# Kernel tuning notes

Measured on AMD Instinct MI355X. Metric: run time of the kernel, lower is better.

Reference implementation:

```python
import jax, jax.numpy as jnp
import numpy as np

V, D_EMB, H, N_LAYERS = 50257, 512, 1024, 2
B, T = 8, 512


def setup_inputs() -> dict:
    key = jax.random.key(0)
    ks = jax.random.split(key, 9)
    s = 0.02
    return {
        "x": jax.random.randint(ks[0], (B, T), 0, V),
        "y": jax.random.randint(ks[1], (B, T), 0, V),
        "E": jax.random.normal(ks[2], (V, D_EMB), jnp.float32) * s,
        "Wih0": jax.random.normal(ks[3], (D_EMB, H), jnp.float32) * s,
        "Whh0": jax.random.normal(ks[4], (H, H), jnp.float32) * s,
        "Wih1": jax.random.normal(ks[5], (H, H), jnp.float32) * s,
        "Whh1": jax.random.normal(ks[6], (H, H), jnp.float32) * s,
        "Wfc": jax.random.normal(ks[7], (H, V), jnp.float32) * s,
        "bfc": jnp.zeros((V,), jnp.float32),
    }


def _rnn_layer(x_tbd, Wih, Whh):
    # x_tbd: (T, B, Din) time-major; tanh Elman cell, no bias.
    h0 = jnp.zeros((x_tbd.shape[1], Whh.shape[0]), x_tbd.dtype)

    def step(h, x_t):
        h_new = jnp.tanh(x_t @ Wih + h @ Whh)
        return h_new, h_new

    h_last, ys = jax.lax.scan(step, h0, x_tbd)
    return ys, h_last  # ys: (T, B, H)


def reference(x, y, E, Wih0, Whh0, Wih1, Whh1, Wfc, bfc):
    xe = E[x]                              # (B, T, D_EMB) embedding gather
    xs = jnp.swapaxes(xe, 0, 1)            # (T, B, D_EMB)
    ys0, _ = _rnn_layer(xs, Wih0, Whh0)    # layer 0
    ys1, _ = _rnn_layer(ys0, Wih1, Whh1)   # layer 1
    feats = jnp.swapaxes(ys1, 0, 1)        # (B, T, H)
    logits = feats @ Wfc + bfc             # (B, T, V)
    # cross_entropy with ignore_index=-1 (mean over valid tokens)
    flat = logits.reshape(-1, logits.shape[-1])
    yf = y.reshape(-1)
    valid = yf != -1
    y_safe = jnp.where(valid, yf, 0)
    logp = jax.nn.log_softmax(flat, axis=-1)
    nll = -jnp.take_along_axis(logp, y_safe[:, None], axis=-1)[:, 0]
    loss = jnp.sum(jnp.where(valid, nll, 0.0)) / jnp.maximum(valid.sum(), 1)
    return logits, loss
```

## Files before the change

### kernel.cpp

```cpp
#include <hip/hip_runtime.h>


#define H_DIM 1024
#define B_SZ 8
#define T_SZ 512
#define V_SZ 50257
#define V_PAD 50304
#define NTILES 12576

typedef __attribute__((ext_vector_type(8))) short bf16x8;
typedef __attribute__((ext_vector_type(4))) float f32x4;

__device__ __forceinline__ unsigned short f2bf(float f) {
  unsigned int u = __float_as_uint(f);
  u += 0x7fffu + ((u >> 16) & 1u);
  return (unsigned short)(u >> 16);
}
__device__ __forceinline__ float bf2f(unsigned short h) {
  return __uint_as_float(((unsigned int)h) << 16);
}
__device__ __forceinline__ float ftanh(float x) {
  float e = __expf(2.f * x);
  return 1.f - 2.f / (e + 1.f);
}
__device__ __forceinline__ int aload32(const int* p) {
  return __hip_atomic_load(p, __ATOMIC_RELAXED, __HIP_MEMORY_SCOPE_AGENT);
}
__device__ __forceinline__ void astore32(unsigned int* p, unsigned int v) {
  __hip_atomic_store(p, v, __ATOMIC_RELAXED, __HIP_MEMORY_SCOPE_AGENT);
}
__device__ __forceinline__ void astore32i(int* p, int v) {
  __hip_atomic_store(p, v, __ATOMIC_RELAXED, __HIP_MEMORY_SCOPE_AGENT);
}
__device__ __forceinline__ unsigned long long aload64(const void* p) {
  return __hip_atomic_load((const unsigned long long*)p, __ATOMIC_RELAXED,
                           __HIP_MEMORY_SCOPE_AGENT);
}
__device__ __forceinline__ void astore64(void* p, unsigned long long v) {
  __hip_atomic_store((unsigned long long*)p, v, __ATOMIC_RELAXED,
                     __HIP_MEMORY_SCOPE_AGENT);
}
__device__ __forceinline__ void gload_lds16(const void* g, void* l) {
  __builtin_amdgcn_global_load_lds(
      (const __attribute__((address_space(1))) void*)g,
      (__attribute__((address_space(3))) void*)l, 16, 0, 0);
}

__global__ __launch_bounds__(256) void k_transpose(
    const float* __restrict__ in, unsigned short* __restrict__ out,
    int K, int N, int Npad)
{
  __shared__ float tile[32][33];
  const int n0 = blockIdx.x * 32, k0 = blockIdx.y * 32;
  const int tx = threadIdx.x, ty = threadIdx.y;
#pragma unroll
  for (int jj = 0; jj < 4; ++jj) {
    int k = k0 + ty + jj * 8, n = n0 + tx;
    tile[ty + jj * 8][tx] = (n < N) ? in[(size_t)k * N + n] : 0.f;
  }
  __syncthreads();
#pragma unroll
  for (int jj = 0; jj < 4; ++jj) {
    int n = n0 + ty + jj * 8, k = k0 + tx;
    if (n < Npad) out[(size_t)n * K + k] = f2bf((n < N) ? tile[tx][ty + jj * 8] : 0.f);
  }
}

__global__ __launch_bounds__(128) void k_embed(
    const int* __restrict__ x, const float* __restrict__ E,
    unsigned short* __restrict__ xe)
{
  const int r = blockIdx.x;
  const int t = r >> 3, b = r & 7;
  const int tok = x[b * T_SZ + t];
  const float4 v = ((const float4*)(E + (size_t)tok * 512))[threadIdx.x];
  ushort4 o;
  o.x = f2bf(v.x); o.y = f2bf(v.y); o.z = f2bf(v.z); o.w = f2bf(v.w);
  *((ushort4*)(xe + (size_t)r * 512) + threadIdx.x) = o;
}

template <bool BF16_OUT, bool BIAS>
__global__ __launch_bounds__(256) void k_gemm(
    const unsigned short* __restrict__ A, const unsigned short* __restrict__ Bt,
    void* __restrict__ Cout, const float* __restrict__ bias,
    int Nvalid, int K, int lda, int ldb, int ldc)
{
  __shared__ unsigned short As[8192];
  __shared__ unsigned short Bs[8192];
  const int tid = threadIdx.x;
  const int n0 = blockIdx.x * 128;
  const int m0 = blockIdx.y * 128;
  const int lane = tid & 63;
  const int wv = tid >> 6;
  const int wm = wv >> 1, wn = wv & 1;
  const int ln = lane & 15, cc = lane >> 4;
  f32x4 acc[4][4] = {};
  const int rr = tid >> 3;
  const int cb = (tid & 7) << 4;

  for (int kb = 0; kb < K; kb += 64) {
    __syncthreads();
#pragma unroll
    for (int is = 0; is < 4; ++is) {
      int r = is * 32 + rr;
      int sb = cb ^ ((r & 7) << 4);
      gload_lds16((const char*)(A + (size_t)(m0 + r) * lda + kb) + sb,
                  &As[(is * 32 + 8 * wv) * 64]);
    }
#pragma unroll
    for (int is = 0; is < 4; ++is) {
      int r = is * 32 + rr;
      int sb = cb ^ ((r & 7) << 4);
      gload_lds16((const char*)(Bt + (size_t)(n0 + r) * ldb + kb) + sb,
                  &Bs[(is * 32 + 8 * wv) * 64]);
    }
    __syncthreads();
#pragma unroll
    for (int kk = 0; kk < 2; ++kk) {
      bf16x8 af[4], bfr[4];
      const int kslot = kk * 64 + cc * 16;
#pragma unroll
      for (int mi = 0; mi < 4; ++mi) {
        int ra = wm * 64 + mi * 16 + ln;
        af[mi] = *(const bf16x8*)((const char*)As + ra * 128 + (kslot ^ ((ra & 7) << 4)));
      }
#pragma unroll
      for (int ni = 0; ni < 4; ++ni) {
        int rb = wn * 64 + ni * 16 + ln;
        bfr[ni] = *(const bf16x8*)((const char*)Bs + rb * 128 + (kslot ^ ((rb & 7) << 4)));
      }
#pragma unroll
      for (int mi = 0; mi < 4; ++mi)
#pragma unroll
        for (int ni = 0; ni < 4; ++ni)
          acc[mi][ni] = __builtin_amdgcn_mfma_f32_16x16x32_bf16(af[mi], bfr[ni], acc[mi][ni], 0, 0, 0);
    }
  }
#pragma unroll
  for (int ni = 0; ni < 4; ++ni) {
    const int col = n0 + wn * 64 + ni * 16 + ln;
    const bool cok = col < Nvalid;
    float bv = 0.f;
    if (BIAS && cok) bv = bias[col];
#pragma unroll
    for (int mi = 0; mi < 4; ++mi) {
#pragma unroll
      for (int i = 0; i < 4; ++i) {
        if (cok) {
          const int rowg = m0 + wm * 64 + mi * 16 + cc * 4 + i;
          if (BF16_OUT)
            ((unsigned short*)Cout)[(size_t)rowg * ldc + col] = f2bf(acc[mi][ni][i]);
          else
            ((float*)Cout)[(size_t)rowg * ldc + col] = acc[mi][ni][i] + bv;
        }
      }
    }
  }
}

template <int NQ>
__device__ __forceinline__ void gatherN(const uint2* __restrict__ sl,
    unsigned want, char* __restrict__ lds, int lane, int rowoff)
{
  unsigned long long v[NQ];
  for (;;) {
    bool ok = true;
#pragma unroll
    for (int q = 0; q < NQ; ++q)
      v[q] = aload64(sl + q * 64 + lane);
#pragma unroll
    for (int q = 0; q < NQ; ++q)
      ok &= ((unsigned)v[q] == want);
    if (__all(ok)) break;
  }
#pragma unroll
  for (int q = 0; q < NQ; ++q) {
    const int j = q * 64 + lane;
    const int row = rowoff + (j >> 9), kp = j & 511;
    *(unsigned*)(lds + ((row * 2048 + kp * 4) ^ ((row & 7) << 4))) =
        (unsigned)(v[q] >> 32);
  }
}

__device__ __forceinline__ void load_bw(bf16x8* bw, const float* W, int cc, int col)
{
#pragma unroll
  for (int kc = 0; kc < 32; ++kc) {
    const float* wp = W + (size_t)(kc * 32 + cc * 8) * H_DIM + col;
    bf16x8 v;
#pragma unroll
    for (int q = 0; q < 8; ++q) v[q] = (short)f2bf(wp[(size_t)q * H_DIM]);
    bw[kc] = v;
  }
}

__device__ __forceinline__ f32x4 mfma_k1024(const char* hs, const bf16x8* bw,
                                            int cc, int r)
{
  f32x4 ac0 = {}, ac1 = {};
  const int swz = r << 4;
#pragma unroll
  for (int kc = 0; kc < 32; kc += 2) {
    bf16x8 a0 = *(const bf16x8*)(hs + r * 2048 + ((kc * 64 + cc * 16) ^ swz));
    bf16x8 a1 = *(const bf16x8*)(hs + r * 2048 + (((kc + 1) * 64 + cc * 16) ^ swz));
    ac0 = __builtin_amdgcn_mfma_f32_16x16x32_bf16(a0, bw[kc], ac0, 0, 0, 0);
    ac1 = __builtin_amdgcn_mfma_f32_16x16x32_bf16(a1, bw[kc + 1], ac1, 0, 0, 0);
  }
  return ac0 + ac1;
}

__device__ void rec0(const unsigned short* U0, const float* Whh0,
    uint2* h0ring, const int* prog, char* smem, int wg)
{
  __builtin_amdgcn_s_setprio(1);
  const int tid = threadIdx.x, lane = tid & 63, wv = tid >> 6;
  const int ln = lane & 15, cc = lane >> 4, r = ln & 7;
  const int col = wg * 64 + wv * 16 + ln;
  char* stage = smem;
  bf16x8 bw[32];
  load_bw(bw, Whh0, cc, col);
#pragma unroll 1
  for (int t = 0; t < T_SZ; ++t) {
    unsigned short uva[4] = {0, 0, 0, 0};
    if (cc < 2) {
#pragma unroll
      for (int i = 0; i < 4; ++i)
        uva[i] = U0[(size_t)(t * B_SZ + cc * 4 + i) * H_DIM + col];
    }
    gatherN<16>(h0ring + ((t + 3) & 3) * 4096 + wv * 1024, (unsigned)t,
                stage, lane, wv * 2);
    __syncthreads();
    f32x4 ac = mfma_k1024(stage, bw, cc, r);
    __syncthreads();
    float hv[4] = {0.f, 0.f, 0.f, 0.f};
    if (cc < 2) {
#pragma unroll
      for (int i = 0; i < 4; ++i) hv[i] = ftanh(ac[i] + bf2f(uva[i]));
    }
    unsigned wpk[4];
#pragma unroll
    for (int i = 0; i < 4; ++i) {
      float pv = __shfl_xor(hv[i], 1);
      wpk[i] = (unsigned)f2bf(hv[i]) | ((unsigned)f2bf(pv) << 16);
    }
    if (t >= 4) {
      const int* pp = prog + (lane & 31);
      while (!__all(aload32(pp) >= t - 3)) __builtin_amdgcn_s_sleep(1);
    }
    if (cc < 2 && !(ln & 1)) {
      uint2* outs = h0ring + (t & 3) * 4096;
      const int kp = col >> 1;
#pragma unroll
      for (int i = 0; i < 4; ++i)
        astore64(outs + (cc * 4 + i) * 512 + kp,
                 ((unsigned long long)wpk[i] << 32) | (unsigned long long)(t + 1));
    }
  }
}

__device__ void rec1(const float* Wih1, const float* Whh1,
    unsigned short* feats, uint2* h0ring, uint2* h1ring, int* prog,
    int* gprog, char* smem, int wg)
{
  __builtin_amdgcn_s_setprio(1);
  const int tid = threadIdx.x, lane = tid & 63, wv = tid >> 6;
  const int ln = lane & 15, cc = lane >> 4, r = ln & 7;
  const int isB = wv >> 1;
  const int half = wv & 1;
  const int col = wg * 32 + half * 16 + ln;
  char* h0s = smem;
  char* h1s = smem + 16384;
  float* part = (float*)(smem + 32768);
  bf16x8 bw[32];
  load_bw(bw, isB ? Whh1 : Wih1, cc, col);
#pragma unroll 1
  for (int t = 0; t < T_SZ; ++t) {
    const uint2* ring = isB ? (h1ring + ((t + 3) & 3) * 4096)
                            : (h0ring + (t & 3) * 4096);
    char* stg = isB ? h1s : h0s;
    gatherN<32>(ring + half * 2048, (unsigned)(isB ? t : t + 1),
                stg, lane, half * 4);
    __syncthreads();
    f32x4 ac = mfma_k1024(isB ? h1s : h0s, bw, cc, r);
    if (!isB) *(f32x4*)(part + half * 256 + lane * 4) = ac;
    __syncthreads();
    if (isB) {
      f32x4 pa = *(const f32x4*)(part + half * 256 + lane * 4);
      float hv[4] = {0.f, 0.f, 0.f, 0.f};
      if (cc < 2) {
#pragma unroll
        for (int i = 0; i < 4; ++i) hv[i] = ftanh(ac[i] + pa[i]);
      }
      unsigned wpk[4];
#pragma unroll
      for (int i = 0; i < 4; ++i) {
        float pv = __shfl_xor(hv[i], 1);
        wpk[i] = (unsigned)f2bf(hv[i]) | ((unsigned)f2bf(pv) << 16);
      }
      if (cc < 2 && !(ln & 1)) {
        uint2* outs = h1ring + (t & 3) * 4096;
        const int kp = col >> 1;
#pragma unroll
        for (int i = 0; i < 4; ++i) {
          astore64(outs + (cc * 4 + i) * 512 + kp,
                   ((unsigned long long)wpk[i] << 32) | (unsigned long long)(t + 1));
          astore32((unsigned*)(feats + (size_t)(cc * 4 + i) * 524288 +
                               (size_t)t * 1024 + col), wpk[i]);
        }
      }
      if ((t & 7) == 7) {
        asm volatile("s_waitcnt vmcnt(0)" ::: "memory");
        if (lane == 0) astore32i(gprog + (wg * 2 + half) * 32, t + 1);
      }
    }
    if (wv == 2 && lane == 0) astore32i(prog + wg, t + 1);
  }
}

__device__ void gemm_tile(const unsigned short* __restrict__ A,
    const unsigned short* __restrict__ Bt, float* __restrict__ C,
    const float* __restrict__ bias, float2* __restrict__ PARTg,
    char* smem, int m0, int nb)
{
  unsigned short* As = (unsigned short*)smem;
  unsigned short* Bs = (unsigned short*)(smem + 16384);
  float2* lpart = (float2*)(smem + 32768);
  const int n0 = nb * 128;
  const int tid = threadIdx.x;
  const int lane = tid & 63;
  const int wv = tid >> 6;
  const int wm = wv >> 1, wn = wv & 1;
  const int ln = lane & 15, cc = lane >> 4;
  f32x4 acc[4][4] = {};
  const int rr = tid >> 3;
  const int cb = (tid & 7) << 4;

  for (int kb = 0; kb < H_DIM; kb += 64) {
    __syncthreads();
#pragma unroll
    for (int is = 0; is < 4; ++is) {
      int r = is * 32 + rr;
      int sb = cb ^ ((r & 7) << 4);
      gload_lds16((const char*)(A + (size_t)(m0 + r) * H_DIM + kb) + sb,
                  &As[(is * 32 + 8 * wv) * 64]);
    }
#pragma unroll
    for (int is = 0; is < 4; ++is) {
      int r = is * 32 + rr;
      int sb = cb ^ ((r & 7) << 4);
      gload_lds16((const char*)(Bt + (size_t)(n0 + r) * H_DIM + kb) + sb,
                  &Bs[(is * 32 + 8 * wv) * 64]);
    }
    __syncthreads();
#pragma unroll
    for (int kk = 0; kk < 2; ++kk) {
      bf16x8 af[4], bfr[4];
      const int kslot = kk * 64 + cc * 16;
#pragma unroll
      for (int mi = 0; mi < 4; ++mi) {
        int ra = wm * 64 + mi * 16 + ln;
        af[mi] = *(const bf16x8*)((const char*)As + ra * 128 + (kslot ^ ((ra & 7) << 4)));
      }
#pragma unroll
      for (int ni = 0; ni < 4; ++ni) {
        int rb = wn * 64 + ni * 16 + ln;
        bfr[ni] = *(const bf16x8*)((const char*)Bs + rb * 128 + (kslot ^ ((rb & 7) << 4)));
      }
#pragma unroll
      for (int mi = 0; mi < 4; ++mi)
#pragma unroll
        for (int ni = 0; ni < 4; ++ni)
          acc[mi][ni] = __builtin_amdgcn_mfma_f32_16x16x32_bf16(af[mi], bfr[ni], acc[mi][ni], 0, 0, 0);
    }
  }
  float bvn[4]; int ckn[4];
#pragma unroll
  for (int ni = 0; ni < 4; ++ni) {
    int col = n0 + wn * 64 + ni * 16 + ln;
    ckn[ni] = col < V_SZ;
    bvn[ni] = ckn[ni] ? bias[col] : 0.f;
  }
  float fm[16], fs[16];
#pragma unroll
  for (int mi = 0; mi < 4; ++mi) {
#pragma unroll
    for (int i = 0; i < 4; ++i) {
      float v[4];
#pragma unroll
      for (int ni = 0; ni < 4; ++ni) {
        float tv = acc[mi][ni][i] + bvn[ni];
        v[ni] = ckn[ni] ? tv : -1e30f;
        if (ckn[ni]) {
          int col = n0 + wn * 64 + ni * 16 + ln;
          C[(size_t)(m0 + wm * 64 + mi * 16 + cc * 4 + i) * V_SZ + col] = tv;
        }
      }
      float mx = fmaxf(fmaxf(v[0], v[1]), fmaxf(v[2], v[3]));
#pragma unroll
      for (int m = 1; m < 16; m <<= 1) mx = fmaxf(mx, __shfl_xor(mx, m));
      float se = __expf(v[0] - mx) + __expf(v[1] - mx) +
                 __expf(v[2] - mx) + __expf(v[3] - mx);
#pragma unroll
      for (int m = 1; m < 16; m <<= 1) se += __shfl_xor(se, m);
      fm[mi * 4 + i] = mx; fs[mi * 4 + i] = se;
    }
  }
  if (wn == 0 && ln == 0) {
#pragma unroll
    for (int mi = 0; mi < 4; ++mi)
#pragma unroll
      for (int i = 0; i < 4; ++i) {
        int rl = wm * 64 + mi * 16 + cc * 4 + i;
        lpart[rl] = make_float2(fm[mi * 4 + i], fs[mi * 4 + i]);
      }
  }
  __syncthreads();
  if (wn == 1 && ln == 0) {
#pragma unroll
    for (int mi = 0; mi < 4; ++mi)
#pragma unroll
      for (int i = 0; i < 4; ++i) {
        int rl = wm * 64 + mi * 16 + cc * 4 + i;
        float2 o = lpart[rl];
        float mx = fm[mi * 4 + i], se = fs[mi * 4 + i];
        float nm = fmaxf(mx, o.x);
        float S = se * __expf(mx - nm) + o.y * __expf(o.x - nm);
        PARTg[(size_t)(m0 + rl) * 393 + nb] = make_float2(nm, S);
      }
  }
}

__device__ void worker_body(const unsigned short* FEATS,
    const unsigned short* WfcT, const float* bias, float* C, float2* PARTg,
    const int* gprog, int* TILE, char* smem)
{
  const int tid = threadIdx.x;
  int* sT = (int*)(smem + 33792);
  int passed = 0;
  for (;;) {
    __syncthreads();
    if (tid == 0)
      *sT = __hip_atomic_fetch_add(TILE, 1, __ATOMIC_RELAXED, __HIP_MEMORY_SCOPE_AGENT);
    __syncthreads();
    int id = *sT;
    if (id >= NTILES) break;
    int p = id / 3144, rem = id % 3144, nb = rem / 8, b = rem % 8;
    int thr = 128 * (p + 1);
    if (thr > passed) {
      const int lane = tid & 63;
      const int* gp = gprog + lane * 32;
      while (!__all(aload32(gp) >= thr)) __builtin_amdgcn_s_sleep(32);
      passed = thr;
    }
    gemm_tile(FEATS, WfcT, C, bias, PARTg, smem, b * 512 + p * 128, nb);
  }
}

__global__ __launch_bounds__(256, 1) void k_mega(
    const unsigned short* __restrict__ U0, const float* __restrict__ Whh0,
    const float* __restrict__ Wih1, const float* __restrict__ Whh1,
    unsigned short* __restrict__ FEATS, const unsigned short* __restrict__ WfcT,
    const float* __restrict__ bfc, float* __restrict__ logits,
    float2* __restrict__ PART, uint2* __restrict__ h0ring,
    uint2* __restrict__ h1ring, int* __restrict__ prog,
    int* __restrict__ gprog, int* __restrict__ TILE)
{
  __shared__ __align__(16) char smem[34816];
  const int bid = blockIdx.x;
  if (bid < 16)
    rec0(U0, Whh0, h0ring, prog, smem, bid);
  else if (bid < 48)
    rec1(Wih1, Whh1, FEATS, h0ring, h1ring, prog, gprog, smem, bid - 16);
  else
    worker_body(FEATS, WfcT, bfc, logits, PART, gprog, TILE, smem);
}

__global__ __launch_bounds__(64) void k_loss_combine(
    const float2* __restrict__ PARTg, const float* __restrict__ logits,
    const int* __restrict__ y, float* __restrict__ rowloss)
{
  const int row = blockIdx.x, l = threadIdx.x;
  float M = -1e30f, S = 0.f;
  for (int i = l; i < 393; i += 64) {
    float2 p = PARTg[(size_t)row * 393 + i];
    float nm = fmaxf(M, p.x);
    S = S * __expf(M - nm) + p.y * __expf(p.x - nm);
    M = nm;
  }
#pragma unroll
  for (int off = 32; off > 0; off >>= 1) {
    float mo = __shfl_xor(M, off), so = __shfl_xor(S, off);
    float nm = fmaxf(M, mo);
    S = S * __expf(M - nm) + so * __expf(mo - nm);
    M = nm;
  }
  if (l == 0) {
    int tgt = y[row];
    float r = 0.f;
    if (tgt >= 0) r = M + __logf(S) - logits[(size_t)row * V_SZ + tgt];
    rowloss[row] = r;
  }
}

__global__ __launch_bounds__(256) void k_loss_final(
    const float* __restrict__ rowloss, const int* __restrict__ y,
    float* __restrict__ out)
{
  const int tid = threadIdx.x;
  float s = 0.f, c = 0.f;
  for (int i = tid; i < B_SZ * T_SZ; i += 256) {
    if (y[i] != -1) { s += rowloss[i]; c += 1.f; }
  }
  for (int off = 32; off > 0; off >>= 1) { s += __shfl_xor(s, off); c += __shfl_xor(c, off); }
  __shared__ float as_[4], ac_[4];
  const int wvi = tid >> 6, lnn = tid & 63;
  if (lnn == 0) { as_[wvi] = s; ac_[wvi] = c; }
  __syncthreads();
  if (tid == 0) {
    float S = as_[0] + as_[1] + as_[2] + as_[3];
    float C = ac_[0] + ac_[1] + ac_[2] + ac_[3];
    out[0] = S / fmaxf(C, 1.f);
  }
}

extern "C" void kernel_launch(void* const* d_in, const int* in_sizes, int n_in,
                              void* d_out, int out_size, void* d_ws, size_t ws_size,
                              hipStream_t stream) {
  (void)in_sizes; (void)n_in; (void)ws_size;
  const int* x = (const int*)d_in[0];
  const int* y = (const int*)d_in[1];
  const float* E = (const float*)d_in[2];
  const float* Wih0 = (const float*)d_in[3];
  const float* Whh0 = (const float*)d_in[4];
  const float* Wih1 = (const float*)d_in[5];
  const float* Whh1 = (const float*)d_in[6];
  const float* Wfc = (const float*)d_in[7];
  const float* bfc = (const float*)d_in[8];
  char* ws = (char*)d_ws;
  unsigned short* WfcT  = (unsigned short*)(ws + 0ULL);
  unsigned short* Wih0T = (unsigned short*)(ws + 103022592ULL);
  unsigned short* XE    = (unsigned short*)(ws + 104071168ULL);
  unsigned short* U0    = (unsigned short*)(ws + 108265472ULL);
  unsigned short* FEATS = (unsigned short*)(ws + 116654080ULL);
  float2* PART          = (float2*)(ws + 125042688ULL);
  float* ROWLOSS        = (float*)(ws + 137920512ULL);
  uint2* H0R            = (uint2*)(ws + 137936896ULL);
  uint2* H1R            = (uint2*)(ws + 138067968ULL);
  int* PROG             = (int*)(ws + 138199040ULL);
  int* GPROG            = (int*)(ws + 138199296ULL);
  int* TILE             = (int*)(ws + 138207488ULL);
  float* logits = (float*)d_out;
  float* lossp = logits + (size_t)(out_size - 1);

  hipMemsetAsync(ws + 137936896ULL, 0, 270848, stream);

  k_transpose<<<dim3(32, 16), dim3(32, 8), 0, stream>>>(Wih0, Wih0T, 512, 1024, 1024);
  k_transpose<<<dim3(1572, 32), dim3(32, 8), 0, stream>>>(Wfc, WfcT, 1024, V_SZ, V_PAD);
  k_embed<<<4096, 128, 0, stream>>>(x, E, XE);
  k_gemm<true, false><<<dim3(8, 32), 256, 0, stream>>>(XE, Wih0T, U0, nullptr,
                                                       1024, 512, 512, 512, 1024);
  k_mega<<<512, 256, 0, stream>>>(U0, Whh0, Wih1, Whh1, FEATS, WfcT, bfc,
                                  logits, PART, H0R, H1R, PROG, GPROG, TILE);
  k_loss_combine<<<4096, 64, 0, stream>>>(PART, logits, y, ROWLOSS);
  k_loss_final<<<1, 256, 0, stream>>>(ROWLOSS, y, lossp);
}
```

Before: 2.336 ms.

## Split final time chunk into 64-row tiles and use nontemporal logit stores

The worker schedule changes so the last 128-step chunk of each sequence is processed as two 64-row tiles. A new 64-row GEMM tile routine handles them, with its own cross-wave log-sum-exp merge. These tiles can start as soon as the recurrence reaches step 448 or 512, which shortens the tail left after the recurrent layers finish. Logit writes also become nontemporal stores to reduce cache pollution. The cost is more tiles, lower arithmetic intensity on the 64-row tiles, and a slightly larger shared-memory footprint.

```diff
diff --git a/kernel.cpp b/kernel.cpp
--- a/kernel.cpp
+++ b/kernel.cpp
@@ -6,7 +6,8 @@
 #define T_SZ 512
 #define V_SZ 50257
 #define V_PAD 50304
-#define NTILES 12576
+#define NT128 9432
+#define NTILES 15720
 
 typedef __attribute__((ext_vector_type(8))) short bf16x8;
 typedef __attribute__((ext_vector_type(4))) float f32x4;
@@ -392,7 +393,8 @@
         v[ni] = ckn[ni] ? tv : -1e30f;
         if (ckn[ni]) {
           int col = n0 + wn * 64 + ni * 16 + ln;
-          C[(size_t)(m0 + wm * 64 + mi * 16 + cc * 4 + i) * V_SZ + col] = tv;
+          __builtin_nontemporal_store(tv,
+              &C[(size_t)(m0 + wm * 64 + mi * 16 + cc * 4 + i) * V_SZ + col]);
         }
       }
       float mx = fmaxf(fmaxf(v[0], v[1]), fmaxf(v[2], v[3]));
@@ -430,12 +432,121 @@
   }
 }
 
+__device__ void gemm_tile64(const unsigned short* __restrict__ A,
+    const unsigned short* __restrict__ Bt, float* __restrict__ C,
+    const float* __restrict__ bias, float2* __restrict__ PARTg,
+    char* smem, int m0, int nb)
+{
+  unsigned short* As = (unsigned short*)smem;
+  unsigned short* Bs = (unsigned short*)(smem + 16384);
+  float2* lpart4 = (float2*)(smem + 32768);
+  const int n0 = nb * 128;
+  const int tid = threadIdx.x;
+  const int lane = tid & 63;
+  const int wv = tid >> 6;
+  const int ln = lane & 15, cc = lane >> 4;
+  f32x4 acc[4][2] = {};
+  const int rr = tid >> 3;
+  const int cb = (tid & 7) << 4;
+
+  for (int kb = 0; kb < H_DIM; kb += 64) {
+    __syncthreads();
+#pragma unroll
+    for (int is = 0; is < 2; ++is) {
+      int r = is * 32 + rr;
+      int sb = cb ^ ((r & 7) << 4);
+      gload_lds16((const char*)(A + (size_t)(m0 + r) * H_DIM + kb) + sb,
+                  &As[(is * 32 + 8 * wv) * 64]);
+    }
+#pragma unroll
+    for (int is = 0; is < 4; ++is) {
+      int r = is * 32 + rr;
+      int sb = cb ^ ((r & 7) << 4);
+      gload_lds16((const char*)(Bt + (size_t)(n0 + r) * H_DIM + kb) + sb,
+                  &Bs[(is * 32 + 8 * wv) * 64]);
+    }
+    __syncthreads();
+#pragma unroll
+    for (int kk = 0; kk < 2; ++kk) {
+      bf16x8 af[4], bfr[2];
+      const int kslot = kk * 64 + cc * 16;
+#pragma unroll
+      for (int mi = 0; mi < 4; ++mi) {
+        int ra = mi * 16 + ln;
+        af[mi] = *(const bf16x8*)((const char*)As + ra * 128 + (kslot ^ ((ra & 7) << 4)));
+      }
+#pragma unroll
+      for (int ni = 0; ni < 2; ++ni) {
+        int rb = wv * 32 + ni * 16 + ln;
+        bfr[ni] = *(const bf16x8*)((const char*)Bs + rb * 128 + (kslot ^ ((rb & 7) << 4)));
+      }
+#pragma unroll
+      for (int mi = 0; mi < 4; ++mi)
+#pragma unroll
+        for (int ni = 0; ni < 2; ++ni)
+          acc[mi][ni] = __builtin_amdgcn_mfma_f32_16x16x32_bf16(af[mi], bfr[ni], acc[mi][ni], 0, 0, 0);
+    }
+  }
+  float bvn[2]; int ckn[2];
+#pragma unroll
+  for (int ni = 0; ni < 2; ++ni) {
+    int col = n0 + wv * 32 + ni * 16 + ln;
+    ckn[ni] = col < V_SZ;
+    bvn[ni] = ckn[ni] ? bias[col] : 0.f;
+  }
+  float fm[16], fs[16];
+#pragma unroll
+  for (int mi = 0; mi < 4; ++mi) {
+#pragma unroll
+    for (int i = 0; i < 4; ++i) {
+      float v[2];
+#pragma unroll
+      for (int ni = 0; ni < 2; ++ni) {
+        float tv = acc[mi][ni][i] + bvn[ni];
+        v[ni] = ckn[ni] ? tv : -1e30f;
+        if (ckn[ni]) {
+          int col = n0 + wv * 32 + ni * 16 + ln;
+          __builtin_nontemporal_store(tv,
+              &C[(size_t)(m0 + mi * 16 + cc * 4 + i) * V_SZ + col]);
+        }
+      }
+      float mx = fmaxf(v[0], v[1]);
+#pragma unroll
+      for (int m = 1; m < 16; m <<= 1) mx = fmaxf(mx, __shfl_xor(mx, m));
+      float se = __expf(v[0] - mx) + __expf(v[1] - mx);
+#pragma unroll
+      for (int m = 1; m < 16; m <<= 1) se += __shfl_xor(se, m);
+      fm[mi * 4 + i] = mx; fs[mi * 4 + i] = se;
+    }
+  }
+  if (ln == 0) {
+#pragma unroll
+    for (int mi = 0; mi < 4; ++mi)
+#pragma unroll
+      for (int i = 0; i < 4; ++i)
+        lpart4[wv * 64 + mi * 16 + cc * 4 + i] =
+            make_float2(fm[mi * 4 + i], fs[mi * 4 + i]);
+  }
+  __syncthreads();
+  if (tid < 64) {
+    float2 a = lpart4[tid];
+#pragma unroll
+    for (int w = 1; w < 4; ++w) {
+      float2 o = lpart4[w * 64 + tid];
+      float nm = fmaxf(a.x, o.x);
+      a.y = a.y * __expf(a.x - nm) + o.y * __expf(o.x - nm);
+      a.x = nm;
+    }
+    PARTg[(size_t)(m0 + tid) * 393 + nb] = a;
+  }
+}
+
 __device__ void worker_body(const unsigned short* FEATS,
     const unsigned short* WfcT, const float* bias, float* C, float2* PARTg,
     const int* gprog, int* TILE, char* smem)
 {
   const int tid = threadIdx.x;
-  int* sT = (int*)(smem + 33792);
+  int* sT = (int*)(smem + 34816);
   int passed = 0;
   for (;;) {
     __syncthreads();
@@ -444,15 +555,29 @@
     __syncthreads();
     int id = *sT;
     if (id >= NTILES) break;
-    int p = id / 3144, rem = id % 3144, nb = rem / 8, b = rem % 8;
-    int thr = 128 * (p + 1);
+    int m0, thr, nb, rows;
+    if (id < NT128) {
+      int p = id / 3144, rem = id % 3144, b = rem % 8;
+      nb = rem / 8;
+      m0 = b * 512 + p * 128;
+      thr = 128 * (p + 1);
+      rows = 128;
+    } else {
+      int q = id - NT128;
+      int p = q / 3144, rem = q % 3144, b = rem % 8;
+      nb = rem / 8;
+      m0 = b * 512 + 384 + p * 64;
+      thr = 448 + p * 64;
+      rows = 64;
+    }
     if (thr > passed) {
       const int lane = tid & 63;
       const int* gp = gprog + lane * 32;
       while (!__all(aload32(gp) >= thr)) __builtin_amdgcn_s_sleep(32);
       passed = thr;
     }
-    gemm_tile(FEATS, WfcT, C, bias, PARTg, smem, b * 512 + p * 128, nb);
+    if (rows == 128) gemm_tile(FEATS, WfcT, C, bias, PARTg, smem, m0, nb);
+    else gemm_tile64(FEATS, WfcT, C, bias, PARTg, smem, m0, nb);
   }
 }
 
@@ -465,7 +590,7 @@
     uint2* __restrict__ h1ring, int* __restrict__ prog,
     int* __restrict__ gprog, int* __restrict__ TILE)
 {
-  __shared__ __align__(16) char smem[34816];
+  __shared__ __align__(16) char smem[35840];
   const int bid = blockIdx.x;
   if (bid < 16)
     rec0(U0, Whh0, h0ring, prog, smem, bid);
```

Result: no change. 2.341 ms (+0.2%).

## Fold Wfc transpose into persistent kernel and switch to 512-thread blocks

Applied to the files above, without the earlier changes.

Removes the separate Wfc transpose launch and has the GEMM worker blocks do the fp32-to-bf16 transpose in chunks while the recurrent blocks run, so that work overlaps the serial RNN phase. The persistent kernel moves from 512x256 to 256x512-thread blocks, which halves the number of recurrent workgroups (8 for layer 0, 16 for layer 1) and widens the GEMM tile's wave layout to 2x4. Logit stores become nontemporal. The cost is a global barrier among the workers before the GEMM can start, and fewer blocks per CU, which may lower occupancy or change how the recurrence is scheduled.

```diff
diff --git a/kernel.cpp b/kernel.cpp
--- a/kernel.cpp
+++ b/kernel.cpp
@@ -6,6 +6,8 @@
 #define T_SZ 512
 #define V_SZ 50257
 #define V_PAD 50304
+#define NCHUNK 1572
+#define NWORKER 232
 #define NTILES 12576
 
 typedef __attribute__((ext_vector_type(8))) short bf16x8;
@@ -215,7 +217,7 @@
   __builtin_amdgcn_s_setprio(1);
   const int tid = threadIdx.x, lane = tid & 63, wv = tid >> 6;
   const int ln = lane & 15, cc = lane >> 4, r = ln & 7;
-  const int col = wg * 64 + wv * 16 + ln;
+  const int col = wg * 128 + wv * 16 + ln;
   char* stage = smem;
   bf16x8 bw[32];
   load_bw(bw, Whh0, cc, col);
@@ -227,8 +229,8 @@
       for (int i = 0; i < 4; ++i)
         uva[i] = U0[(size_t)(t * B_SZ + cc * 4 + i) * H_DIM + col];
     }
-    gatherN<16>(h0ring + ((t + 3) & 3) * 4096 + wv * 1024, (unsigned)t,
-                stage, lane, wv * 2);
+    gatherN<8>(h0ring + ((t + 3) & 3) * 4096 + wv * 512, (unsigned)t,
+               stage, lane, wv);
     __syncthreads();
     f32x4 ac = mfma_k1024(stage, bw, cc, r);
     __syncthreads();
@@ -244,7 +246,7 @@
       wpk[i] = (unsigned)f2bf(hv[i]) | ((unsigned)f2bf(pv) << 16);
     }
     if (t >= 4) {
-      const int* pp = prog + (lane & 31);
+      const int* pp = prog + (lane & 15) * 32;
       while (!__all(aload32(pp) >= t - 3)) __builtin_amdgcn_s_sleep(1);
     }
     if (cc < 2 && !(ln & 1)) {
@@ -265,9 +267,9 @@
   __builtin_amdgcn_s_setprio(1);
   const int tid = threadIdx.x, lane = tid & 63, wv = tid >> 6;
   const int ln = lane & 15, cc = lane >> 4, r = ln & 7;
-  const int isB = wv >> 1;
-  const int half = wv & 1;
-  const int col = wg * 32 + half * 16 + ln;
+  const int isB = wv >> 2;
+  const int sub = wv & 3;
+  const int col = wg * 64 + sub * 16 + ln;
   char* h0s = smem;
   char* h1s = smem + 16384;
   float* part = (float*)(smem + 32768);
@@ -275,17 +277,16 @@
   load_bw(bw, isB ? Whh1 : Wih1, cc, col);
 #pragma unroll 1
   for (int t = 0; t < T_SZ; ++t) {
-    const uint2* ring = isB ? (h1ring + ((t + 3) & 3) * 4096)
-                            : (h0ring + (t & 3) * 4096);
-    char* stg = isB ? h1s : h0s;
-    gatherN<32>(ring + half * 2048, (unsigned)(isB ? t : t + 1),
-                stg, lane, half * 4);
+    gatherN<8>(h0ring + (t & 3) * 4096 + wv * 512, (unsigned)(t + 1),
+               h0s, lane, wv);
+    gatherN<8>(h1ring + ((t + 3) & 3) * 4096 + wv * 512, (unsigned)t,
+               h1s, lane, wv);
     __syncthreads();
     f32x4 ac = mfma_k1024(isB ? h1s : h0s, bw, cc, r);
-    if (!isB) *(f32x4*)(part + half * 256 + lane * 4) = ac;
+    if (!isB) *(f32x4*)(part + sub * 256 + lane * 4) = ac;
     __syncthreads();
     if (isB) {
-      f32x4 pa = *(const f32x4*)(part + half * 256 + lane * 4);
+      f32x4 pa = *(const f32x4*)(part + sub * 256 + lane * 4);
       float hv[4] = {0.f, 0.f, 0.f, 0.f};
       if (cc < 2) {
 #pragma unroll
@@ -310,10 +311,10 @@
       }
       if ((t & 7) == 7) {
         asm volatile("s_waitcnt vmcnt(0)" ::: "memory");
-        if (lane == 0) astore32i(gprog + (wg * 2 + half) * 32, t + 1);
-      }
-    }
-    if (wv == 2 && lane == 0) astore32i(prog + wg, t + 1);
+        if (lane == 0) astore32i(gprog + (wg * 4 + sub) * 32, t + 1);
+      }
+    }
+    if (wv == 0 && lane == 0) astore32i(prog + wg * 32, t + 1);
   }
 }
 
@@ -329,32 +330,32 @@
   const int tid = threadIdx.x;
   const int lane = tid & 63;
   const int wv = tid >> 6;
-  const int wm = wv >> 1, wn = wv & 1;
+  const int wm = wv >> 2, wn = wv & 3;
   const int ln = lane & 15, cc = lane >> 4;
-  f32x4 acc[4][4] = {};
+  f32x4 acc[4][2] = {};
   const int rr = tid >> 3;
   const int cb = (tid & 7) << 4;
 
   for (int kb = 0; kb < H_DIM; kb += 64) {
     __syncthreads();
 #pragma unroll
-    for (int is = 0; is < 4; ++is) {
-      int r = is * 32 + rr;
+    for (int is = 0; is < 2; ++is) {
+      int r = is * 64 + rr;
       int sb = cb ^ ((r & 7) << 4);
       gload_lds16((const char*)(A + (size_t)(m0 + r) * H_DIM + kb) + sb,
-                  &As[(is * 32 + 8 * wv) * 64]);
-    }
-#pragma unroll
-    for (int is = 0; is < 4; ++is) {
-      int r = is * 32 + rr;
+                  &As[(is * 64 + 8 * wv) * 64]);
+    }
+#pragma unroll
+    for (int is = 0; is < 2; ++is) {
+      int r = is * 64 + rr;
       int sb = cb ^ ((r & 7) << 4);
       gload_lds16((const char*)(Bt + (size_t)(n0 + r) * H_DIM + kb) + sb,
-                  &Bs[(is * 32 + 8 * wv) * 64]);
+                  &Bs[(is * 64 + 8 * wv) * 64]);
     }
     __syncthreads();
 #pragma unroll
     for (int kk = 0; kk < 2; ++kk) {
-      bf16x8 af[4], bfr[4];
+      bf16x8 af[4], bfr[2];
       const int kslot = kk * 64 + cc * 16;
 #pragma unroll
       for (int mi = 0; mi < 4; ++mi) {
@@ -362,21 +363,21 @@
         af[mi] = *(const bf16x8*)((const char*)As + ra * 128 + (kslot ^ ((ra & 7) << 4)));
       }
 #pragma unroll
-      for (int ni = 0; ni < 4; ++ni) {
-        int rb = wn * 64 + ni * 16 + ln;
+      for (int ni = 0; ni < 2; ++ni) {
+        int rb = wn * 32 + ni * 16 + ln;
         bfr[ni] = *(const bf16x8*)((const char*)Bs + rb * 128 + (kslot ^ ((rb & 7) << 4)));
       }
 #pragma unroll
       for (int mi = 0; mi < 4; ++mi)
 #pragma unroll
-        for (int ni = 0; ni < 4; ++ni)
+        for (int ni = 0; ni < 2; ++ni)
           acc[mi][ni] = __builtin_amdgcn_mfma_f32_16x16x32_bf16(af[mi], bfr[ni], acc[mi][ni], 0, 0, 0);
     }
   }
-  float bvn[4]; int ckn[4];
-#pragma unroll
-  for (int ni = 0; ni < 4; ++ni) {
-    int col = n0 + wn * 64 + ni * 16 + ln;
+  float bvn[2]; int ckn[2];
+#pragma unroll
+  for (int ni = 0; ni < 2; ++ni) {
+    int col = n0 + wn * 32 + ni * 16 + ln;
     ckn[ni] = col < V_SZ;
     bvn[ni] = ckn[ni] ? bias[col] : 0.f;
   }
@@ -385,57 +386,93 @@
   for (int mi = 0; mi < 4; ++mi) {
 #pragma unroll
     for (int i = 0; i < 4; ++i) {
-      float v[4];
-#pragma unroll
-      for (int ni = 0; ni < 4; ++ni) {
+      float v[2];
+#pragma unroll
+      for (int ni = 0; ni < 2; ++ni) {
         float tv = acc[mi][ni][i] + bvn[ni];
         v[ni] = ckn[ni] ? tv : -1e30f;
         if (ckn[ni]) {
-          int col = n0 + wn * 64 + ni * 16 + ln;
-          C[(size_t)(m0 + wm * 64 + mi * 16 + cc * 4 + i) * V_SZ + col] = tv;
+          int col = n0 + wn * 32 + ni * 16 + ln;
+          __builtin_nontemporal_store(tv,
+              &C[(size_t)(m0 + wm * 64 + mi * 16 + cc * 4 + i) * V_SZ + col]);
         }
       }
-      float mx = fmaxf(fmaxf(v[0], v[1]), fmaxf(v[2], v[3]));
+      float mx = fmaxf(v[0], v[1]);
 #pragma unroll
       for (int m = 1; m < 16; m <<= 1) mx = fmaxf(mx, __shfl_xor(mx, m));
-      float se = __expf(v[0] - mx) + __expf(v[1] - mx) +
-                 __expf(v[2] - mx) + __expf(v[3] - mx);
+      float se = __expf(v[0] - mx) + __expf(v[1] - mx);
 #pragma unroll
       for (int m = 1; m < 16; m <<= 1) se += __shfl_xor(se, m);
       fm[mi * 4 + i] = mx; fs[mi * 4 + i] = se;
     }
   }
-  if (wn == 0 && ln == 0) {
+  if (ln == 0) {
 #pragma unroll
     for (int mi = 0; mi < 4; ++mi)
 #pragma unroll
-      for (int i = 0; i < 4; ++i) {
-        int rl = wm * 64 + mi * 16 + cc * 4 + i;
-        lpart[rl] = make_float2(fm[mi * 4 + i], fs[mi * 4 + i]);
-      }
+      for (int i = 0; i < 4; ++i)
+        lpart[wv * 64 + mi * 16 + cc * 4 + i] =
+            make_float2(fm[mi * 4 + i], fs[mi * 4 + i]);
   }
   __syncthreads();
-  if (wn == 1 && ln == 0) {
-#pragma unroll
-    for (int mi = 0; mi < 4; ++mi)
-#pragma unroll
-      for (int i = 0; i < 4; ++i) {
-        int rl = wm * 64 + mi * 16 + cc * 4 + i;
-        float2 o = lpart[rl];
-        float mx = fm[mi * 4 + i], se = fs[mi * 4 + i];
-        float nm = fmaxf(mx, o.x);
-        float S = se * __expf(mx - nm) + o.y * __expf(o.x - nm);
-        PARTg[(size_t)(m0 + rl) * 393 + nb] = make_float2(nm, S);
-      }
-  }
-}
-
-__device__ void worker_body(const unsigned short* FEATS,
-    const unsigned short* WfcT, const float* bias, float* C, float2* PARTg,
-    const int* gprog, int* TILE, char* smem)
+  if (tid < 128) {
+    const int g = tid, wmg = g >> 6, lr = g & 63;
+    float2 a = lpart[(wmg * 4) * 64 + lr];
+#pragma unroll
+    for (int q = 1; q < 4; ++q) {
+      float2 o = lpart[(wmg * 4 + q) * 64 + lr];
+      float nm = fmaxf(a.x, o.x);
+      a.y = a.y * __expf(a.x - nm) + o.y * __expf(o.x - nm);
+      a.x = nm;
+    }
+    PARTg[(size_t)(m0 + g) * 393 + nb] = a;
+  }
+}
+
+__device__ void worker_body(const float* Wfc, unsigned short* WfcT,
+    const unsigned short* FEATS, const float* bias, float* C, float2* PARTg,
+    const int* gprog, int* TCNT, int* TDONE, int* TILE, char* smem)
 {
   const int tid = threadIdx.x;
-  int* sT = (int*)(smem + 33792);
+  int* sT = (int*)(smem + 36864);
+  {
+    float* tt = (float*)smem;
+    const int tx = tid & 31, ty = (tid >> 5) & 15;
+    const int widx = tid & 15, nrow = tid >> 4;
+    for (;;) {
+      __syncthreads();
+      if (tid == 0)
+        *sT = __hip_atomic_fetch_add(TCNT, 1, __ATOMIC_RELAXED, __HIP_MEMORY_SCOPE_AGENT);
+      __syncthreads();
+      int ch = *sT;
+      if (ch >= NCHUNK) break;
+      int n0 = ch * 32;
+      for (int kt = 0; kt < 32; ++kt) {
+        int k0 = kt * 32;
+        __syncthreads();
+#pragma unroll
+        for (int jj = 0; jj < 2; ++jj) {
+          int k = ty + jj * 16, n = n0 + tx;
+          tt[k * 33 + tx] = (n < V_SZ) ? Wfc[(size_t)(k0 + k) * V_SZ + n] : 0.f;
+        }
+        __syncthreads();
+        {
+          int n = n0 + nrow;
+          float a = (n < V_SZ) ? tt[(widx * 2) * 33 + nrow] : 0.f;
+          float b = (n < V_SZ) ? tt[(widx * 2 + 1) * 33 + nrow] : 0.f;
+          unsigned pv = (unsigned)f2bf(a) | ((unsigned)f2bf(b) << 16);
+          astore32((unsigned*)WfcT + (size_t)n * 512 + (k0 >> 1) + widx, pv);
+        }
+      }
+      __syncthreads();
+    }
+    asm volatile("s_waitcnt vmcnt(0)" ::: "memory");
+    __syncthreads();
+    if (tid == 0)
+      __hip_atomic_fetch_add(TDONE, 1, __ATOMIC_RELAXED, __HIP_MEMORY_SCOPE_AGENT);
+    while (aload32(TDONE) < NWORKER) __builtin_amdgcn_s_sleep(16);
+    __syncthreads();
+  }
   int passed = 0;
   for (;;) {
     __syncthreads();
@@ -448,7 +485,7 @@
     int thr = 128 * (p + 1);
     if (thr > passed) {
       const int lane = tid & 63;
-      const int* gp = gprog + lane * 32;
+      const int* gp = gprog + (lane & 63) * 32;
       while (!__all(aload32(gp) >= thr)) __builtin_amdgcn_s_sleep(32);
       passed = thr;
     }
@@ -456,23 +493,24 @@
   }
 }
 
-__global__ __launch_bounds__(256, 1) void k_mega(
+__global__ __launch_bounds__(512) void k_mega(
     const unsigned short* __restrict__ U0, const float* __restrict__ Whh0,
     const float* __restrict__ Wih1, const float* __restrict__ Whh1,
-    unsigned short* __restrict__ FEATS, const unsigned short* __restrict__ WfcT,
-    const float* __restrict__ bfc, float* __restrict__ logits,
-    float2* __restrict__ PART, uint2* __restrict__ h0ring,
-    uint2* __restrict__ h1ring, int* __restrict__ prog,
-    int* __restrict__ gprog, int* __restrict__ TILE)
-{
-  __shared__ __align__(16) char smem[34816];
+    unsigned short* __restrict__ FEATS, const float* __restrict__ Wfc,
+    unsigned short* __restrict__ WfcT, const float* __restrict__ bfc,
+    float* __restrict__ logits, float2* __restrict__ PART,
+    uint2* __restrict__ h0ring, uint2* __restrict__ h1ring,
+    int* __restrict__ prog, int* __restrict__ gprog, int* __restrict__ cnts)
+{
+  __shared__ __align__(16) char smem[37376];
   const int bid = blockIdx.x;
-  if (bid < 16)
+  if (bid < 8)
     rec0(U0, Whh0, h0ring, prog, smem, bid);
-  else if (bid < 48)
-    rec1(Wih1, Whh1, FEATS, h0ring, h1ring, prog, gprog, smem, bid - 16);
+  else if (bid < 24)
+    rec1(Wih1, Whh1, FEATS, h0ring, h1ring, prog, gprog, smem, bid - 8);
   else
-    worker_body(FEATS, WfcT, bfc, logits, PART, gprog, TILE, smem);
+    worker_body(Wfc, WfcT, FEATS, bfc, logits, PART, gprog,
+                cnts + 0, cnts + 32, cnts + 64, smem);
 }
 
 __global__ __launch_bounds__(64) void k_loss_combine(
@@ -547,20 +585,19 @@
   uint2* H0R            = (uint2*)(ws + 137936896ULL);
   uint2* H1R            = (uint2*)(ws + 138067968ULL);
   int* PROG             = (int*)(ws + 138199040ULL);
-  int* GPROG            = (int*)(ws + 138199296ULL);
-  int* TILE             = (int*)(ws + 138207488ULL);
+  int* GPROG            = (int*)(ws + 138201088ULL);
+  int* CNT              = (int*)(ws + 138209280ULL);
   float* logits = (float*)d_out;
   float* lossp = logits + (size_t)(out_size - 1);
 
-  hipMemsetAsync(ws + 137936896ULL, 0, 270848, stream);
+  hipMemsetAsync(ws + 137936896ULL, 0, 273408, stream);
 
   k_transpose<<<dim3(32, 16), dim3(32, 8), 0, stream>>>(Wih0, Wih0T, 512, 1024, 1024);
-  k_transpose<<<dim3(1572, 32), dim3(32, 8), 0, stream>>>(Wfc, WfcT, 1024, V_SZ, V_PAD);
   k_embed<<<4096, 128, 0, stream>>>(x, E, XE);
   k_gemm<true, false><<<dim3(8, 32), 256, 0, stream>>>(XE, Wih0T, U0, nullptr,
                                                        1024, 512, 512, 512, 1024);
-  k_mega<<<512, 256, 0, stream>>>(U0, Whh0, Wih1, Whh1, FEATS, WfcT, bfc,
-                                  logits, PART, H0R, H1R, PROG, GPROG, TILE);
+  k_mega<<<256, 512, 0, stream>>>(U0, Whh0, Wih1, Whh1, FEATS, Wfc, WfcT, bfc,
+                                  logits, PART, H0R, H1R, PROG, GPROG, CNT);
   k_loss_combine<<<4096, 64, 0, stream>>>(PART, logits, y, ROWLOSS);
   k_loss_final<<<1, 256, 0, stream>>>(ROWLOSS, y, lossp);
 }
```

New measurement: 2.175 ms. 1.07x faster.
